# Kernel optimization log

Measured on AMD Instinct MI355X. Metric: run time of the kernel, lower is better.

The kernel has to match this reference:

```python
import jax, jax.numpy as jnp
import numpy as np

NUM_NODES = 500000
NUM_RELATIONS = 500
HIDDEN = 128
R_DIM = 64
BATCH = 65536
EPS = 1e-12


def setup_inputs() -> dict:
    key = jax.random.key(0)
    k1, k2, k3, k4, k5, k6 = jax.random.split(key, 6)
    return {
        "src": jax.random.randint(k1, (BATCH,), 0, NUM_NODES, dtype=jnp.int32),
        "rel": jax.random.randint(k2, (BATCH,), 0, NUM_RELATIONS, dtype=jnp.int32),
        "dst": jax.random.randint(k3, (BATCH,), 0, NUM_NODES, dtype=jnp.int32),
        "entity_embedding": jax.random.normal(k4, (NUM_NODES, HIDDEN), dtype=jnp.float32),
        "relation_embedding": jax.random.normal(k5, (NUM_RELATIONS, R_DIM), dtype=jnp.float32),
        "projection_matrix": jax.random.normal(k6, (NUM_RELATIONS, HIDDEN, R_DIM), dtype=jnp.float32),
    }


def _l2_normalize(x):
    # F.normalize(p=2): x / max(||x||, eps)
    n = jnp.sqrt(jnp.sum(x * x, axis=-1, keepdims=True))
    return x / jnp.maximum(n, EPS)


def reference(src, rel, dst, entity_embedding, relation_embedding, projection_matrix):
    src_emb = entity_embedding[src]            # [B, H]
    dst_emb = entity_embedding[dst]            # [B, H]
    rel_emb = relation_embedding[rel]          # [B, R]
    proj = projection_matrix[rel]              # [B, H, R] per-relation gather
    src_proj = jnp.einsum("bh,bhr->br", src_emb, proj)
    dst_proj = jnp.einsum("bh,bhr->br", dst_emb, proj)
    src_proj = _l2_normalize(src_proj)
    dst_proj = _l2_normalize(dst_proj)
    diff = src_proj + rel_emb - dst_proj
    score = jnp.sqrt(jnp.sum(diff * diff, axis=-1))  # [B]
    return score
```

## Files before the change

### kernel.cpp

```cpp
#include <hip/hip_runtime.h>
#include <math.h>

#define BATCH   65536
#define NREL    500
#define HIDDEN  128
#define RDIM    64
#define EPS     1e-12f
#define SPLIT   2
#define NBLK    256

#define WS_BH     0
#define WS_TOT    128000
#define WS_OFF    128512
#define WS_IT     131072
#define WS_S      196608
#define WS_D      262144

__device__ __forceinline__ unsigned short f2bf(float x) {
    unsigned u = __float_as_uint(x);
    u += 0x7fffu + ((u >> 16) & 1u);
    return (unsigned short)(u >> 16);
}

__global__ void histA_k(const int* __restrict__ rel, unsigned* __restrict__ bh) {
    __shared__ unsigned lh[NREL];
    int tid = threadIdx.x;
    for (int i = tid; i < NREL; i += 256) lh[i] = 0u;
    __syncthreads();
    int r = rel[blockIdx.x * 256 + tid];
    atomicAdd(&lh[r], 1u);
    __syncthreads();
    for (int i = tid; i < NREL; i += 256) bh[i * NBLK + blockIdx.x] = lh[i];
}

__global__ void scanB1_k(unsigned* __restrict__ bh, unsigned* __restrict__ tot) {
    int t = blockIdx.x * 256 + threadIdx.x;
    if (t >= NREL) return;
    unsigned run = 0;
    unsigned* row = bh + (size_t)t * NBLK;
    for (int b = 0; b < NBLK; b++) {
        unsigned x = row[b];
        row[b] = run;
        run += x;
    }
    tot[t] = run;
}

__global__ void scanB2_k(const unsigned* __restrict__ tot, unsigned* __restrict__ off) {
    __shared__ unsigned sA[512], sB[512];
    int t = threadIdx.x;
    unsigned v = (t < NREL) ? tot[t] : 0u;
    sA[t] = v;
    __syncthreads();
    unsigned* cur = sA;
    unsigned* nxt = sB;
    for (int d = 1; d < 512; d <<= 1) {
        unsigned x = cur[t];
        if (t >= d) x += cur[t - d];
        nxt[t] = x;
        __syncthreads();
        unsigned* tmp = cur; cur = nxt; nxt = tmp;
    }
    unsigned incl = cur[t];
    unsigned excl = incl - v;
    if (t < NREL)  off[t] = excl;
    if (t == NREL) off[t] = incl;
}

__global__ void scatC_k(const int* __restrict__ rel,
                        const int* __restrict__ src,
                        const int* __restrict__ dst,
                        const unsigned* __restrict__ off,
                        const unsigned* __restrict__ bh,
                        unsigned* __restrict__ sIt,
                        int* __restrict__ sS,
                        int* __restrict__ sD) {
    __shared__ unsigned lbase[NREL];
    __shared__ unsigned lcnt[NREL];
    int tid = threadIdx.x;
    for (int i = tid; i < NREL; i += 256) {
        lbase[i] = off[i] + bh[i * NBLK + blockIdx.x];
        lcnt[i] = 0u;
    }
    __syncthreads();
    int item = blockIdx.x * 256 + tid;
    int r = rel[item];
    unsigned p = lbase[r] + atomicAdd(&lcnt[r], 1u);
    sIt[p] = (unsigned)item;
    sS[p] = src[item];
    sD[p] = dst[item];
}

__global__ __launch_bounds__(256, 4) void proc_k(
        const float*    __restrict__ ent,
        const float*    __restrict__ relemb,
        const float*    __restrict__ proj,
        const unsigned* __restrict__ off,
        const unsigned* __restrict__ sIt,
        const int*      __restrict__ sS,
        const int*      __restrict__ sD,
        float*          __restrict__ out) {
    __shared__ unsigned short Pb[(HIDDEN / 8) * RDIM * 8];
    __shared__ float SD[4][2][HIDDEN][4];
    __shared__ float Rlds[RDIM];

    const int tid  = threadIdx.x;
    const int w    = tid >> 6;
    const int lane = tid & 63;
    const int rblk = blockIdx.x / SPLIT;
    const int part = blockIdx.x % SPLIT;

    const unsigned start = off[rblk];
    const unsigned end   = off[rblk + 1];
    const unsigned cnt   = end - start;

    const float* Pg = proj + (size_t)rblk * (HIDDEN * RDIM);
    for (int f = tid; f < (HIDDEN * RDIM) / 4; f += 256) {
        float4 v = ((const float4*)Pg)[f];
        int h  = f >> 4;
        int r0 = (f & 15) << 2;
        int c  = h >> 3, k = h & 7;
        Pb[(c * RDIM + r0 + 0) * 8 + k] = f2bf(v.x);
        Pb[(c * RDIM + r0 + 1) * 8 + k] = f2bf(v.y);
        Pb[(c * RDIM + r0 + 2) * 8 + k] = f2bf(v.z);
        Pb[(c * RDIM + r0 + 3) * 8 + k] = f2bf(v.w);
    }
    if (tid < RDIM) Rlds[tid] = relemb[rblk * RDIM + tid];

    const int half = tid >> 7;
    const int hh   = tid & 127;
    const int ntiles = (int)((cnt + 15u) >> 4);

    float pv[16];

    if (part < ntiles) {
        unsigned base = start + ((unsigned)part << 4);
        const int* nodes = half ? sD : sS;
        #pragma unroll
        for (int i = 0; i < 16; i++) {
            unsigned p = base + (unsigned)i;
            if (p >= end) p = end - 1;
            int n = nodes[p];
            pv[i] = ent[(size_t)n * HIDDEN + hh];
        }
    }

    for (int t = part; t < ntiles; t += SPLIT) {
        const unsigned base = start + ((unsigned)t << 4);
        __syncthreads();

        #pragma unroll
        for (int q = 0; q < 4; q++) {
            *(float4*)&SD[q][half][hh][0] =
                make_float4(pv[q * 4 + 0], pv[q * 4 + 1], pv[q * 4 + 2], pv[q * 4 + 3]);
        }
        __syncthreads();

        if (t + SPLIT < ntiles) {
            unsigned nb = start + ((unsigned)(t + SPLIT) << 4);
            const int* nodes = half ? sD : sS;
            #pragma unroll
            for (int i = 0; i < 16; i++) {
                unsigned p = nb + (unsigned)i;
                if (p >= end) p = end - 1;
                int n = nodes[p];
                pv[i] = ent[(size_t)n * HIDDEN + hh];
            }
        }

        float as0 = 0.f, as1 = 0.f, as2 = 0.f, as3 = 0.f;
        float ad0 = 0.f, ad1 = 0.f, ad2 = 0.f, ad3 = 0.f;
        #pragma unroll 4
        for (int c = 0; c < HIDDEN / 8; c++) {
            uint4 pu = *(const uint4*)&Pb[(c * RDIM + lane) * 8];
            #pragma unroll
            for (int k = 0; k < 8; k++) {
                unsigned word = (k < 2) ? pu.x : (k < 4) ? pu.y : (k < 6) ? pu.z : pu.w;
                float p = (k & 1) ? __uint_as_float(word & 0xffff0000u)
                                  : __uint_as_float(word << 16);
                int h = c * 8 + k;
                float4 s = *(const float4*)&SD[w][0][h][0];
                float4 d = *(const float4*)&SD[w][1][h][0];
                as0 = fmaf(s.x, p, as0);
                as1 = fmaf(s.y, p, as1);
                as2 = fmaf(s.z, p, as2);
                as3 = fmaf(s.w, p, as3);
                ad0 = fmaf(d.x, p, ad0);
                ad1 = fmaf(d.y, p, ad1);
                ad2 = fmaf(d.z, p, ad2);
                ad3 = fmaf(d.w, p, ad3);
            }
        }

        const float relv = Rlds[lane];
        float As[4] = {as0, as1, as2, as3};
        float Ad[4] = {ad0, ad1, ad2, ad3};
        #pragma unroll
        for (int j = 0; j < 4; j++) {
            float ss = As[j] * As[j];
            float dd = Ad[j] * Ad[j];
            #pragma unroll
            for (int m = 1; m < 64; m <<= 1) {
                ss += __shfl_xor(ss, m, 64);
                dd += __shfl_xor(dd, m, 64);
            }
            float ns = fmaxf(sqrtf(ss), EPS);
            float nd = fmaxf(sqrtf(dd), EPS);
            float diff = As[j] / ns + relv - Ad[j] / nd;
            float sc = diff * diff;
            #pragma unroll
            for (int m = 1; m < 64; m <<= 1) {
                sc += __shfl_xor(sc, m, 64);
            }
            unsigned p = base + (unsigned)((w << 2) + j);
            if (lane == 0 && p < end) {
                out[sIt[p]] = sqrtf(sc);
            }
        }
    }
}

extern "C" void kernel_launch(void* const* d_in, const int* in_sizes, int n_in,
                              void* d_out, int out_size, void* d_ws, size_t ws_size,
                              hipStream_t stream) {
    (void)in_sizes; (void)n_in; (void)out_size; (void)ws_size;
    const int*   src    = (const int*)d_in[0];
    const int*   rel    = (const int*)d_in[1];
    const int*   dst    = (const int*)d_in[2];
    const float* ent    = (const float*)d_in[3];
    const float* relemb = (const float*)d_in[4];
    const float* proj   = (const float*)d_in[5];
    float*       out    = (float*)d_out;

    unsigned* ws  = (unsigned*)d_ws;
    unsigned* bh  = ws + WS_BH;
    unsigned* tot = ws + WS_TOT;
    unsigned* off = ws + WS_OFF;
    unsigned* sIt = ws + WS_IT;
    int*      sS  = (int*)(ws + WS_S);
    int*      sD  = (int*)(ws + WS_D);

    histA_k <<<NBLK, 256, 0, stream>>>(rel, bh);
    scanB1_k<<<2, 256, 0, stream>>>(bh, tot);
    scanB2_k<<<1, 512, 0, stream>>>(tot, off);
    scatC_k <<<NBLK, 256, 0, stream>>>(rel, src, dst, off, bh, sIt, sS, sD);
    proc_k  <<<NREL * SPLIT, 256, 0, stream>>>(ent, relemb, proj, off, sIt, sS, sD, out);
}
```

Measured before the change: 403.4 us.

## Use bf16 MFMA for per-relation projection and wave-parallel bucket scan

The projection kernel now converts gathered entity rows to bf16 in shared memory and computes the projections with 16x16x32 bf16 MFMA instructions instead of scalar FMAs. This processes 32 items per tile with interleaved src/dst rows. The register prefetch of the next tile is dropped, so gathers are no longer overlapped with compute. The per-relation block-offset scan now uses one wave per relation with shuffle scans instead of a serial loop per thread. Rounding entity values to bf16 adds precision loss.

```diff
diff --git a/kernel.cpp b/kernel.cpp
--- a/kernel.cpp
+++ b/kernel.cpp
@@ -16,6 +16,9 @@
 #define WS_S      196608
 #define WS_D      262144
 
+typedef __attribute__((ext_vector_type(8))) short short8;
+typedef __attribute__((ext_vector_type(4))) float f32x4;
+
 __device__ __forceinline__ unsigned short f2bf(float x) {
     unsigned u = __float_as_uint(x);
     u += 0x7fffu + ((u >> 16) & 1u);
@@ -34,16 +37,24 @@
 }
 
 __global__ void scanB1_k(unsigned* __restrict__ bh, unsigned* __restrict__ tot) {
-    int t = blockIdx.x * 256 + threadIdx.x;
-    if (t >= NREL) return;
+    int wv   = (blockIdx.x * 256 + threadIdx.x) >> 6;
+    int lane = threadIdx.x & 63;
+    if (wv >= NREL) return;
+    unsigned* row = bh + (size_t)wv * NBLK;
     unsigned run = 0;
-    unsigned* row = bh + (size_t)t * NBLK;
-    for (int b = 0; b < NBLK; b++) {
-        unsigned x = row[b];
-        row[b] = run;
-        run += x;
-    }
-    tot[t] = run;
+    #pragma unroll
+    for (int c = 0; c < NBLK; c += 64) {
+        unsigned v = row[c + lane];
+        unsigned x = v;
+        #pragma unroll
+        for (int m = 1; m < 64; m <<= 1) {
+            unsigned y = __shfl_up(x, m, 64);
+            if (lane >= m) x += y;
+        }
+        row[c + lane] = run + x - v;
+        run += __shfl(x, 63, 64);
+    }
+    if (lane == 0) tot[wv] = run;
 }
 
 __global__ void scanB2_k(const unsigned* __restrict__ tot, unsigned* __restrict__ off) {
@@ -100,8 +111,8 @@
         const int*      __restrict__ sS,
         const int*      __restrict__ sD,
         float*          __restrict__ out) {
-    __shared__ unsigned short Pb[(HIDDEN / 8) * RDIM * 8];
-    __shared__ float SD[4][2][HIDDEN][4];
+    __shared__ __align__(16) short Pt[RDIM][136];
+    __shared__ __align__(16) short Ab[64][136];
     __shared__ float Rlds[RDIM];
 
     const int tid  = threadIdx.x;
@@ -114,108 +125,100 @@
     const unsigned end   = off[rblk + 1];
     const unsigned cnt   = end - start;
 
-    const float* Pg = proj + (size_t)rblk * (HIDDEN * RDIM);
+    const float4* Pg4 = (const float4*)(proj + (size_t)rblk * (HIDDEN * RDIM));
     for (int f = tid; f < (HIDDEN * RDIM) / 4; f += 256) {
-        float4 v = ((const float4*)Pg)[f];
+        float4 v = Pg4[f];
         int h  = f >> 4;
         int r0 = (f & 15) << 2;
-        int c  = h >> 3, k = h & 7;
-        Pb[(c * RDIM + r0 + 0) * 8 + k] = f2bf(v.x);
-        Pb[(c * RDIM + r0 + 1) * 8 + k] = f2bf(v.y);
-        Pb[(c * RDIM + r0 + 2) * 8 + k] = f2bf(v.z);
-        Pb[(c * RDIM + r0 + 3) * 8 + k] = f2bf(v.w);
+        Pt[r0 + 0][h] = (short)f2bf(v.x);
+        Pt[r0 + 1][h] = (short)f2bf(v.y);
+        Pt[r0 + 2][h] = (short)f2bf(v.z);
+        Pt[r0 + 3][h] = (short)f2bf(v.w);
     }
     if (tid < RDIM) Rlds[tid] = relemb[rblk * RDIM + tid];
 
-    const int half = tid >> 7;
-    const int hh   = tid & 127;
-    const int ntiles = (int)((cnt + 15u) >> 4);
-
-    float pv[16];
-
-    if (part < ntiles) {
-        unsigned base = start + ((unsigned)part << 4);
-        const int* nodes = half ? sD : sS;
-        #pragma unroll
-        for (int i = 0; i < 16; i++) {
-            unsigned p = base + (unsigned)i;
+    if (cnt == 0) return;
+
+    const int r_   = tid >> 2;
+    const int qq   = tid & 3;
+    const int sitm = r_ >> 1;
+    const int* nodes = (r_ & 1) ? sD : sS;
+
+    const int c    = lane & 15;
+    const int g    = lane >> 4;
+    const int q8   = g * 8;
+    const int arow = (w << 4) + c;
+
+    const int nst = (int)((cnt + 31u) >> 5);
+    for (int t = part; t < nst; t += SPLIT) {
+        const unsigned base = start + ((unsigned)t << 5);
+        __syncthreads();
+
+        {
+            unsigned p = base + (unsigned)sitm;
             if (p >= end) p = end - 1;
             int n = nodes[p];
-            pv[i] = ent[(size_t)n * HIDDEN + hh];
-        }
-    }
-
-    for (int t = part; t < ntiles; t += SPLIT) {
-        const unsigned base = start + ((unsigned)t << 4);
+            const float4* eg = (const float4*)(ent + (size_t)n * HIDDEN + qq * 32);
+            unsigned buf[16];
+            #pragma unroll
+            for (int j = 0; j < 8; j++) {
+                float4 v = eg[j];
+                buf[2 * j]     = ((unsigned)f2bf(v.y) << 16) | f2bf(v.x);
+                buf[2 * j + 1] = ((unsigned)f2bf(v.w) << 16) | f2bf(v.z);
+            }
+            uint4* dstp = (uint4*)&Ab[r_][qq * 32];
+            #pragma unroll
+            for (int s = 0; s < 4; s++) dstp[s] = ((uint4*)buf)[s];
+        }
         __syncthreads();
 
-        #pragma unroll
-        for (int q = 0; q < 4; q++) {
-            *(float4*)&SD[q][half][hh][0] =
-                make_float4(pv[q * 4 + 0], pv[q * 4 + 1], pv[q * 4 + 2], pv[q * 4 + 3]);
-        }
-        __syncthreads();
-
-        if (t + SPLIT < ntiles) {
-            unsigned nb = start + ((unsigned)(t + SPLIT) << 4);
-            const int* nodes = half ? sD : sS;
-            #pragma unroll
-            for (int i = 0; i < 16; i++) {
-                unsigned p = nb + (unsigned)i;
-                if (p >= end) p = end - 1;
-                int n = nodes[p];
-                pv[i] = ent[(size_t)n * HIDDEN + hh];
+        f32x4 acc[4];
+        #pragma unroll
+        for (int nt = 0; nt < 4; nt++) acc[nt] = (f32x4){0.f, 0.f, 0.f, 0.f};
+
+        #pragma unroll
+        for (int kk = 0; kk < 4; kk++) {
+            short8 af = *(const short8*)&Ab[arow][kk * 32 + q8];
+            #pragma unroll
+            for (int nt = 0; nt < 4; nt++) {
+                short8 bf = *(const short8*)&Pt[nt * 16 + c][kk * 32 + q8];
+                acc[nt] = __builtin_amdgcn_mfma_f32_16x16x32_bf16(af, bf, acc[nt], 0, 0, 0);
             }
         }
 
-        float as0 = 0.f, as1 = 0.f, as2 = 0.f, as3 = 0.f;
-        float ad0 = 0.f, ad1 = 0.f, ad2 = 0.f, ad3 = 0.f;
-        #pragma unroll 4
-        for (int c = 0; c < HIDDEN / 8; c++) {
-            uint4 pu = *(const uint4*)&Pb[(c * RDIM + lane) * 8];
-            #pragma unroll
-            for (int k = 0; k < 8; k++) {
-                unsigned word = (k < 2) ? pu.x : (k < 4) ? pu.y : (k < 6) ? pu.z : pu.w;
-                float p = (k & 1) ? __uint_as_float(word & 0xffff0000u)
-                                  : __uint_as_float(word << 16);
-                int h = c * 8 + k;
-                float4 s = *(const float4*)&SD[w][0][h][0];
-                float4 d = *(const float4*)&SD[w][1][h][0];
-                as0 = fmaf(s.x, p, as0);
-                as1 = fmaf(s.y, p, as1);
-                as2 = fmaf(s.z, p, as2);
-                as3 = fmaf(s.w, p, as3);
-                ad0 = fmaf(d.x, p, ad0);
-                ad1 = fmaf(d.y, p, ad1);
-                ad2 = fmaf(d.z, p, ad2);
-                ad3 = fmaf(d.w, p, ad3);
-            }
-        }
-
-        const float relv = Rlds[lane];
-        float As[4] = {as0, as1, as2, as3};
-        float Ad[4] = {ad0, ad1, ad2, ad3};
+        float ssq[4];
         #pragma unroll
         for (int j = 0; j < 4; j++) {
-            float ss = As[j] * As[j];
-            float dd = Ad[j] * Ad[j];
-            #pragma unroll
-            for (int m = 1; m < 64; m <<= 1) {
-                ss += __shfl_xor(ss, m, 64);
-                dd += __shfl_xor(dd, m, 64);
-            }
-            float ns = fmaxf(sqrtf(ss), EPS);
-            float nd = fmaxf(sqrtf(dd), EPS);
-            float diff = As[j] / ns + relv - Ad[j] / nd;
-            float sc = diff * diff;
-            #pragma unroll
-            for (int m = 1; m < 64; m <<= 1) {
-                sc += __shfl_xor(sc, m, 64);
-            }
-            unsigned p = base + (unsigned)((w << 2) + j);
-            if (lane == 0 && p < end) {
-                out[sIt[p]] = sqrtf(sc);
-            }
+            ssq[j] = acc[0][j] * acc[0][j] + acc[1][j] * acc[1][j]
+                   + acc[2][j] * acc[2][j] + acc[3][j] * acc[3][j];
+        }
+        #pragma unroll
+        for (int m = 1; m < 16; m <<= 1) {
+            #pragma unroll
+            for (int j = 0; j < 4; j++) ssq[j] += __shfl_xor(ssq[j], m, 64);
+        }
+        float inv[4];
+        #pragma unroll
+        for (int j = 0; j < 4; j++) inv[j] = 1.0f / fmaxf(sqrtf(ssq[j]), EPS);
+
+        float sa = 0.f, sb = 0.f;
+        #pragma unroll
+        for (int nt = 0; nt < 4; nt++) {
+            float rv = Rlds[nt * 16 + c];
+            float da = acc[nt][0] * inv[0] + rv - acc[nt][1] * inv[1];
+            float db = acc[nt][2] * inv[2] + rv - acc[nt][3] * inv[3];
+            sa = fmaf(da, da, sa);
+            sb = fmaf(db, db, sb);
+        }
+        #pragma unroll
+        for (int m = 1; m < 16; m <<= 1) {
+            sa += __shfl_xor(sa, m, 64);
+            sb += __shfl_xor(sb, m, 64);
+        }
+        if (c == 0) {
+            unsigned pa = base + (unsigned)((w << 3) + (g << 1));
+            if (pa < end)     out[sIt[pa]]     = sqrtf(sa);
+            if (pa + 1 < end) out[sIt[pa + 1]] = sqrtf(sb);
         }
     }
 }
@@ -241,7 +244,7 @@
     int*      sD  = (int*)(ws + WS_D);
 
     histA_k <<<NBLK, 256, 0, stream>>>(rel, bh);
-    scanB1_k<<<2, 256, 0, stream>>>(bh, tot);
+    scanB1_k<<<125, 256, 0, stream>>>(bh, tot);
     scanB2_k<<<1, 512, 0, stream>>>(tot, off);
     scatC_k <<<NBLK, 256, 0, stream>>>(rel, src, dst, off, bh, sIt, sS, sD);
     proc_k  <<<NREL * SPLIT, 256, 0, stream>>>(ent, relemb, proj, off, sIt, sS, sD, out);
```

Result: faster. 337.6 us (-16.3%).
